# Kernel optimization log

Measured on AMD Instinct MI355X. Metric: run time of the kernel, lower is better.

The kernel has to match this reference:

```python
import jax, jax.numpy as jnp
import numpy as np

N = 20480      # total nodes
E = 327680     # total edges (avg degree 16)
B = 16         # graphs in batch
IN = 16        # node feature dim
H = 8          # hidden_out_channel
CO = 64        # conv_out_channel
ET = 36        # n_edge_types
EF = 2         # edge_features
OUT = 1        # classifier out
DIMS = [(IN, H), (H, H), (H, H), (H, CO)]


def setup_inputs() -> dict:
    key = jax.random.key(0)
    ks = jax.random.split(key, 32)
    inp = {}
    inp['x'] = jax.random.normal(ks[0], (N, IN), jnp.float32)
    inp['edge_index'] = jax.random.randint(ks[1], (2, E), 0, N)
    inp['edge_type'] = jax.random.randint(ks[2], (E,), 0, ET)
    inp['edge_attr'] = jax.random.normal(ks[3], (E, EF), jnp.float32)
    inp['cell_type'] = jax.random.randint(ks[4], (N,), 0, 2)
    inp['batch'] = (jnp.arange(N) // (N // B)).astype(jnp.int32)
    i = 5
    for l, (ci, co) in enumerate(DIMS, 1):
        d = ci * co
        s = 1.0 / np.sqrt(EF)
        inp[f'emb{l}'] = jax.random.normal(ks[i], (ET, d), jnp.float32) * 0.02; i += 1
        inp[f'wh{l}'] = jax.random.normal(ks[i], (EF, d), jnp.float32) * s; i += 1
        inp[f'bh{l}'] = jnp.zeros((d,), jnp.float32)
        inp[f'wg{l}'] = jax.random.normal(ks[i], (EF, d), jnp.float32) * s; i += 1
        inp[f'bg{l}'] = jnp.zeros((d,), jnp.float32)
        inp[f'root{l}'] = jax.random.normal(ks[i], (ci, co), jnp.float32) / np.sqrt(ci); i += 1
        inp[f'bias{l}'] = jnp.zeros((co,), jnp.float32)
    inp['clf_w'] = jax.random.normal(ks[i], (CO, OUT), jnp.float32) / np.sqrt(CO)
    inp['clf_b'] = jnp.zeros((OUT,), jnp.float32)
    return inp


def edge_weights(etype, ef, emb, wh, bh, wg, bg):
    # EdgeNN: relu(embedding(type) * fc_h(feat) + fc_g(feat)) -> [E, cin*cout]
    return jax.nn.relu(emb[etype] * (ef @ wh + bh) + (ef @ wg + bg))


def nnconv(h, src, dst, W, root, bias):
    # NNConv(aggr='mean', root_weight=True): gather src feats, per-edge matmul, scatter-mean
    cin, cout = root.shape
    msg = jnp.einsum('ei,eio->eo', h[src], W.reshape(-1, cin, cout))  # [E, cout]
    agg = jax.ops.segment_sum(msg, dst, num_segments=N)
    deg = jax.ops.segment_sum(jnp.ones_like(msg[:, 0]), dst, num_segments=N)
    return agg / jnp.maximum(deg, 1.0)[:, None] + h @ root + bias


def reference(x, edge_index, edge_type, edge_attr, cell_type, batch,
              emb1, wh1, bh1, wg1, bg1, root1, bias1,
              emb2, wh2, bh2, wg2, bg2, root2, bias2,
              emb3, wh3, bh3, wg3, bg3, root3, bias3,
              emb4, wh4, bh4, wg4, bg4, root4, bias4,
              clf_w, clf_b):
    src, dst = edge_index[0], edge_index[1]
    layers = [(emb1, wh1, bh1, wg1, bg1, root1, bias1),
              (emb2, wh2, bh2, wg2, bg2, root2, bias2),
              (emb3, wh3, bh3, wg3, bg3, root3, bias3),
              (emb4, wh4, bh4, wg4, bg4, root4, bias4)]
    h = x
    for (emb, wh, bh, wg, bg, root, bias) in layers:  # fixed 4 structurally-distinct layers
        W = edge_weights(edge_type, edge_attr, emb, wh, bh, wg, bg)
        h = jax.nn.relu(nnconv(h, src, dst, W, root, bias))
    # gated scatter-mean pooling over tumor cells (cell_type == 1)
    gate = (cell_type == 1).astype(jnp.int32)
    seg = gate * (batch.astype(jnp.int32) + 1)  # 0 = masked-out bucket
    pooled = jax.ops.segment_sum(h, seg, num_segments=B + 1)
    cnt = jax.ops.segment_sum(jnp.ones((h.shape[0],), h.dtype), seg, num_segments=B + 1)
    pooled = (pooled / jnp.maximum(cnt, 1.0)[:, None])[1:B + 1]  # [B, CO]
    return jax.nn.sigmoid(pooled @ clf_w + clf_b)  # hazards [B, OUT]
```

## Files before the change

### kernel.cpp

```cpp
#include <hip/hip_runtime.h>
#include <math.h>

#define NN 20480
#define NE 327680
#define NBATCH 16

typedef float v2f __attribute__((ext_vector_type(2)));

#if __has_builtin(__builtin_elementwise_max)
#define VMAX0(a) __builtin_elementwise_max((a), (v2f){0.f, 0.f})
#else
static __device__ __forceinline__ v2f VMAX0(v2f a) {
  v2f r; r.x = fmaxf(a.x, 0.f); r.y = fmaxf(a.y, 0.f); return r;
}
#endif

__global__ void hist_kernel(const int* __restrict__ dst, int* __restrict__ cnt) {
  int e = blockIdx.x * blockDim.x + threadIdx.x;
  if (e < NE) atomicAdd(&cnt[dst[e]], 1);
}

__global__ __launch_bounds__(1024) void scan_kernel(const int* __restrict__ cnt,
                                                    int* __restrict__ off,
                                                    int* __restrict__ cur) {
  __shared__ int part[1024];
  int tid = threadIdx.x;
  const int PT = NN / 1024;
  int loc[PT];
  int run = 0;
  int base = tid * PT;
#pragma unroll
  for (int k = 0; k < PT; k++) { loc[k] = run; run += cnt[base + k]; }
  part[tid] = run;
  __syncthreads();
  for (int d = 1; d < 1024; d <<= 1) {
    int t = (tid >= d) ? part[tid - d] : 0;
    __syncthreads();
    part[tid] += t;
    __syncthreads();
  }
  int pre = (tid == 0) ? 0 : part[tid - 1];
#pragma unroll
  for (int k = 0; k < PT; k++) {
    off[base + k] = pre + loc[k];
    cur[base + k] = pre + loc[k];
  }
  if (tid == 1023) off[NN] = pre + run;
}

__global__ void scatter_kernel(const int* __restrict__ src, const int* __restrict__ dst,
                               const int* __restrict__ etype, const float* __restrict__ eattr,
                               int* __restrict__ cur, float4* __restrict__ es) {
  int e = blockIdx.x * blockDim.x + threadIdx.x;
  if (e >= NE) return;
  int d = dst[e];
  int pos = atomicAdd(&cur[d], 1);
  es[pos] = make_float4(__int_as_float(src[e]), __int_as_float(etype[e]),
                        eattr[2 * e], eattr[2 * e + 1]);
}

__global__ __launch_bounds__(256) void transpose_kernel(
    const float* __restrict__ e1, const float* __restrict__ e2,
    const float* __restrict__ e3, const float* __restrict__ e4,
    float* __restrict__ t1, float* __restrict__ t2,
    float* __restrict__ t3, float* __restrict__ t4) {
  int idx = blockIdx.x * 256 + threadIdx.x;
  if (idx < 36 * 128) {
    int t = idx >> 7, r = idx & 127, o = r >> 4, i = r & 15;
    t1[idx] = e1[(t << 7) + i * 8 + o];
  }
  if (idx < 36 * 64) {
    int t = idx >> 6, r = idx & 63, o = r >> 3, i = r & 7;
    t2[idx] = e2[(t << 6) + i * 8 + o];
    t3[idx] = e3[(t << 6) + i * 8 + o];
  }
  {
    int t = idx >> 9, r = idx & 511, o = r >> 3, i = r & 7;
    t4[idx] = e4[(t << 9) + i * 64 + o];
  }
}

__global__ __launch_bounds__(256) void layer_small16(
    const int* __restrict__ off, const float4* __restrict__ es,
    const float* __restrict__ h_in, const float* __restrict__ embT,
    const float* __restrict__ wh, const float* __restrict__ bh,
    const float* __restrict__ wg, const float* __restrict__ bg,
    const float* __restrict__ root, const float* __restrict__ bias,
    float* __restrict__ h_out) {
  constexpr int D = 128;
  int lane = threadIdx.x & 63;
  int o = lane & 7;
  int ihalf = (lane >> 3) & 1;
  int esub = lane >> 4;
  int ibase = ihalf * 8;
  v2f rwh0[4], rwh1[4], rbh[4], rwg0[4], rwg1[4], rbg[4], rroot[4];
#pragma unroll
  for (int p = 0; p < 4; p++) {
    int a = (ibase + 2 * p) * 8 + o, b = (ibase + 2 * p + 1) * 8 + o;
    rwh0[p] = (v2f){wh[a], wh[b]};
    rwh1[p] = (v2f){wh[D + a], wh[D + b]};
    rbh[p]  = (v2f){bh[a], bh[b]};
    rwg0[p] = (v2f){wg[a], wg[b]};
    rwg1[p] = (v2f){wg[D + a], wg[D + b]};
    rbg[p]  = (v2f){bg[a], bg[b]};
    rroot[p] = (v2f){root[a], root[b]};
  }
  float rbias = bias[o];
  int n = __builtin_amdgcn_readfirstlane((int)(blockIdx.x * 4) + (int)(threadIdx.x >> 6));
  int beg = off[n], end = off[n + 1];
  int nIter = (end - beg + 3) >> 2;
  float acc = 0.f;
  int j = beg + esub;
  bool val0 = j < end;
  float4 rec0 = val0 ? es[j] : make_float4(0.f, 0.f, 0.f, 0.f);
  int s0 = __float_as_int(rec0.x);
  const float4* hp0 = (const float4*)(h_in + s0 * 16 + ibase);
  float4 hA0 = hp0[0], hB0 = hp0[1];
  for (int it = 0; it < nIter; ++it) {
    int j1 = j + 4;
    bool val1 = j1 < end;
    float4 rec1 = val1 ? es[j1] : make_float4(0.f, 0.f, 0.f, 0.f);
    int s1 = __float_as_int(rec1.x);
    const float4* hp1 = (const float4*)(h_in + s1 * 16 + ibase);
    float4 hA1 = hp1[0], hB1 = hp1[1];
    int t0 = __float_as_int(rec0.y);
    const float4* sp = (const float4*)(embT + t0 * 128 + o * 16 + ibase);
    float4 sv0 = sp[0], sv1 = sp[1];
    v2f stv[4] = {(v2f){sv0.x, sv0.y}, (v2f){sv0.z, sv0.w},
                  (v2f){sv1.x, sv1.y}, (v2f){sv1.z, sv1.w}};
    v2f hv[4] = {(v2f){hA0.x, hA0.y}, (v2f){hA0.z, hA0.w},
                 (v2f){hB0.x, hB0.y}, (v2f){hB0.z, hB0.w}};
    v2f ef0 = (v2f){rec0.z, rec0.z}, ef1 = (v2f){rec0.w, rec0.w};
    v2f msg = {0.f, 0.f};
#pragma unroll
    for (int p = 0; p < 4; p++) {
      v2f hval = ef0 * rwh0[p] + ef1 * rwh1[p] + rbh[p];
      v2f gval = ef0 * rwg0[p] + ef1 * rwg1[p] + rbg[p];
      msg += hv[p] * VMAX0(stv[p] * hval + gval);
    }
    acc += val0 ? (msg.x + msg.y) : 0.f;
    rec0 = rec1; hA0 = hA1; hB0 = hB1; val0 = val1; j = j1;
  }
  acc += __shfl_xor(acc, 8);
  acc += __shfl_xor(acc, 16);
  acc += __shfl_xor(acc, 32);
  const float* hn = h_in + n * 16 + ibase;
  v2f rtv = {0.f, 0.f};
#pragma unroll
  for (int p = 0; p < 4; p++)
    rtv += (v2f){hn[2 * p], hn[2 * p + 1]} * rroot[p];
  float rt = rtv.x + rtv.y;
  rt += __shfl_xor(rt, 8);
  float deg = (float)(end - beg);
  float val = fmaxf(rbias + rt + acc / fmaxf(deg, 1.f), 0.f);
  if (lane < 8) h_out[n * 8 + o] = val;
}

__global__ __launch_bounds__(256) void layer_small8(
    const int* __restrict__ off, const float4* __restrict__ es,
    const float* __restrict__ h_in, const float* __restrict__ embT,
    const float* __restrict__ wh, const float* __restrict__ bh,
    const float* __restrict__ wg, const float* __restrict__ bg,
    const float* __restrict__ root, const float* __restrict__ bias,
    float* __restrict__ h_out) {
  int lane = threadIdx.x & 63;
  int o = lane & 7, esub = lane >> 3;
  v2f rwh0[4], rwh1[4], rbh[4], rwg0[4], rwg1[4], rbg[4], rroot[4];
#pragma unroll
  for (int p = 0; p < 4; p++) {
    int a = (2 * p) * 8 + o, b = (2 * p + 1) * 8 + o;
    rwh0[p] = (v2f){wh[a], wh[b]};
    rwh1[p] = (v2f){wh[64 + a], wh[64 + b]};
    rbh[p]  = (v2f){bh[a], bh[b]};
    rwg0[p] = (v2f){wg[a], wg[b]};
    rwg1[p] = (v2f){wg[64 + a], wg[64 + b]};
    rbg[p]  = (v2f){bg[a], bg[b]};
    rroot[p] = (v2f){root[a], root[b]};
  }
  float rbias = bias[o];
  int n = __builtin_amdgcn_readfirstlane((int)(blockIdx.x * 4) + (int)(threadIdx.x >> 6));
  int beg = off[n], end = off[n + 1];
  int nIter = (end - beg + 7) >> 3;
  float acc = 0.f;
  int j = beg + esub;
  bool val0 = j < end;
  float4 rec0 = val0 ? es[j] : make_float4(0.f, 0.f, 0.f, 0.f);
  int s0 = __float_as_int(rec0.x);
  const float4* hp0 = (const float4*)(h_in + s0 * 8);
  float4 hA0 = hp0[0], hB0 = hp0[1];
  for (int it = 0; it < nIter; ++it) {
    int j1 = j + 8;
    bool val1 = j1 < end;
    float4 rec1 = val1 ? es[j1] : make_float4(0.f, 0.f, 0.f, 0.f);
    int s1 = __float_as_int(rec1.x);
    const float4* hp1 = (const float4*)(h_in + s1 * 8);
    float4 hA1 = hp1[0], hB1 = hp1[1];
    int t0 = __float_as_int(rec0.y);
    const float4* sp = (const float4*)(embT + t0 * 64 + o * 8);
    float4 sv0 = sp[0], sv1 = sp[1];
    v2f stv[4] = {(v2f){sv0.x, sv0.y}, (v2f){sv0.z, sv0.w},
                  (v2f){sv1.x, sv1.y}, (v2f){sv1.z, sv1.w}};
    v2f hv[4] = {(v2f){hA0.x, hA0.y}, (v2f){hA0.z, hA0.w},
                 (v2f){hB0.x, hB0.y}, (v2f){hB0.z, hB0.w}};
    v2f ef0 = (v2f){rec0.z, rec0.z}, ef1 = (v2f){rec0.w, rec0.w};
    v2f msg = {0.f, 0.f};
#pragma unroll
    for (int p = 0; p < 4; p++) {
      v2f hval = ef0 * rwh0[p] + ef1 * rwh1[p] + rbh[p];
      v2f gval = ef0 * rwg0[p] + ef1 * rwg1[p] + rbg[p];
      msg += hv[p] * VMAX0(stv[p] * hval + gval);
    }
    acc += val0 ? (msg.x + msg.y) : 0.f;
    rec0 = rec1; hA0 = hA1; hB0 = hB1; val0 = val1; j = j1;
  }
  acc += __shfl_xor(acc, 8);
  acc += __shfl_xor(acc, 16);
  acc += __shfl_xor(acc, 32);
  const float* hn = h_in + n * 8;
  v2f rtv = {0.f, 0.f};
#pragma unroll
  for (int p = 0; p < 4; p++)
    rtv += (v2f){hn[2 * p], hn[2 * p + 1]} * rroot[p];
  float deg = (float)(end - beg);
  float val = fmaxf(rbias + rtv.x + rtv.y + acc / fmaxf(deg, 1.f), 0.f);
  if (lane < 8) h_out[n * 8 + o] = val;
}

__global__ __launch_bounds__(256) void layer_l4(
    const int* __restrict__ off, const float4* __restrict__ es,
    const float* __restrict__ h_in, const float* __restrict__ embT,
    const float* __restrict__ wh, const float* __restrict__ bh,
    const float* __restrict__ wg, const float* __restrict__ bg,
    const float* __restrict__ root, const float* __restrict__ bias,
    float* __restrict__ h_out) {
  int lane = threadIdx.x & 63;
  v2f rwh0[4], rwh1[4], rbh[4], rwg0[4], rwg1[4], rbg[4], rroot[4];
#pragma unroll
  for (int p = 0; p < 4; p++) {
    int a = (2 * p) * 64 + lane, b = (2 * p + 1) * 64 + lane;
    rwh0[p] = (v2f){wh[a], wh[b]};
    rwh1[p] = (v2f){wh[512 + a], wh[512 + b]};
    rbh[p]  = (v2f){bh[a], bh[b]};
    rwg0[p] = (v2f){wg[a], wg[b]};
    rwg1[p] = (v2f){wg[512 + a], wg[512 + b]};
    rbg[p]  = (v2f){bg[a], bg[b]};
    rroot[p] = (v2f){root[a], root[b]};
  }
  float rbias = bias[lane];
  int n = __builtin_amdgcn_readfirstlane((int)(blockIdx.x * 4) + (int)(threadIdx.x >> 6));
  int beg = off[n], end = off[n + 1];
  float acc0 = 0.f, acc1 = 0.f;
  int e = beg;
  for (; e + 2 <= end; e += 2) {
    float4 r0 = es[e], r1 = es[e + 1];
    int s0 = __float_as_int(r0.x), t0 = __float_as_int(r0.y);
    int s1 = __float_as_int(r1.x), t1 = __float_as_int(r1.y);
    const float4* hp0 = (const float4*)(h_in + s0 * 8);
    const float4* hp1 = (const float4*)(h_in + s1 * 8);
    float4 a0 = hp0[0], a1 = hp0[1];
    float4 b0 = hp1[0], b1 = hp1[1];
    const float4* ep0 = (const float4*)(embT + t0 * 512 + lane * 8);
    const float4* ep1 = (const float4*)(embT + t1 * 512 + lane * 8);
    float4 s00 = ep0[0], s01 = ep0[1];
    float4 s10 = ep1[0], s11 = ep1[1];
    v2f sv0[4] = {(v2f){s00.x, s00.y}, (v2f){s00.z, s00.w},
                  (v2f){s01.x, s01.y}, (v2f){s01.z, s01.w}};
    v2f sv1[4] = {(v2f){s10.x, s10.y}, (v2f){s10.z, s10.w},
                  (v2f){s11.x, s11.y}, (v2f){s11.z, s11.w}};
    v2f hva[4] = {(v2f){a0.x, a0.y}, (v2f){a0.z, a0.w},
                  (v2f){a1.x, a1.y}, (v2f){a1.z, a1.w}};
    v2f hvb[4] = {(v2f){b0.x, b0.y}, (v2f){b0.z, b0.w},
                  (v2f){b1.x, b1.y}, (v2f){b1.z, b1.w}};
    v2f e00 = (v2f){r0.z, r0.z}, e01 = (v2f){r0.w, r0.w};
    v2f e10 = (v2f){r1.z, r1.z}, e11 = (v2f){r1.w, r1.w};
    v2f m0 = {0.f, 0.f}, m1 = {0.f, 0.f};
#pragma unroll
    for (int p = 0; p < 4; p++) {
      v2f hv0 = e00 * rwh0[p] + e01 * rwh1[p] + rbh[p];
      v2f gv0 = e00 * rwg0[p] + e01 * rwg1[p] + rbg[p];
      m0 += hva[p] * VMAX0(sv0[p] * hv0 + gv0);
      v2f hv1 = e10 * rwh0[p] + e11 * rwh1[p] + rbh[p];
      v2f gv1 = e10 * rwg0[p] + e11 * rwg1[p] + rbg[p];
      m1 += hvb[p] * VMAX0(sv1[p] * hv1 + gv1);
    }
    acc0 += m0.x + m0.y;
    acc1 += m1.x + m1.y;
  }
  if (e < end) {
    float4 r0 = es[e];
    int s0 = __float_as_int(r0.x), t0 = __float_as_int(r0.y);
    const float4* hp0 = (const float4*)(h_in + s0 * 8);
    float4 a0 = hp0[0], a1 = hp0[1];
    const float4* ep0 = (const float4*)(embT + t0 * 512 + lane * 8);
    float4 s00 = ep0[0], s01 = ep0[1];
    v2f sv0[4] = {(v2f){s00.x, s00.y}, (v2f){s00.z, s00.w},
                  (v2f){s01.x, s01.y}, (v2f){s01.z, s01.w}};
    v2f hva[4] = {(v2f){a0.x, a0.y}, (v2f){a0.z, a0.w},
                  (v2f){a1.x, a1.y}, (v2f){a1.z, a1.w}};
    v2f e00 = (v2f){r0.z, r0.z}, e01 = (v2f){r0.w, r0.w};
    v2f m0 = {0.f, 0.f};
#pragma unroll
    for (int p = 0; p < 4; p++) {
      v2f hv0 = e00 * rwh0[p] + e01 * rwh1[p] + rbh[p];
      v2f gv0 = e00 * rwg0[p] + e01 * rwg1[p] + rbg[p];
      m0 += hva[p] * VMAX0(sv0[p] * hv0 + gv0);
    }
    acc0 += m0.x + m0.y;
  }
  float acc = acc0 + acc1;
  float deg = (float)(end - beg);
  const float* hn = h_in + n * 8;
  v2f rtv = {0.f, 0.f};
#pragma unroll
  for (int p = 0; p < 4; p++)
    rtv += (v2f){hn[2 * p], hn[2 * p + 1]} * rroot[p];
  h_out[n * 64 + lane] = fmaxf(rbias + rtv.x + rtv.y + acc / fmaxf(deg, 1.f), 0.f);
}

__global__ __launch_bounds__(256) void pool1_kernel(
    const float* __restrict__ h4, const int* __restrict__ ct,
    float* __restrict__ pooled, float* __restrict__ pcnt) {
  __shared__ float ss[4][64];
  __shared__ float sc[4];
  int b = blockIdx.x / 20, c = blockIdx.x % 20;
  int base = b * (NN / NBATCH) + c * 64;
  int o = threadIdx.x & 63, sub = threadIdx.x >> 6;
  float sum = 0.f, cnt = 0.f;
  for (int j = sub; j < 64; j += 4) {
    int n = base + j;
    if (ct[n] == 1) { sum += h4[n * 64 + o]; cnt += 1.f; }
  }
  ss[sub][o] = sum;
  if (o == 0) sc[sub] = cnt;
  __syncthreads();
  if (threadIdx.x < 64) {
    float tot = ss[0][o] + ss[1][o] + ss[2][o] + ss[3][o];
    unsafeAtomicAdd(&pooled[b * 64 + o], tot);
    if (o == 0) unsafeAtomicAdd(&pcnt[b], sc[0] + sc[1] + sc[2] + sc[3]);
  }
}

__global__ __launch_bounds__(1024) void pool2_kernel(
    const float* __restrict__ pooled, const float* __restrict__ pcnt,
    const float* __restrict__ clf_w, const float* __restrict__ clf_b,
    float* __restrict__ out) {
  int b = threadIdx.x >> 6, o = threadIdx.x & 63;
  float c = pcnt[b];
  float v = (pooled[b * 64 + o] / fmaxf(c, 1.f)) * clf_w[o];
#pragma unroll
  for (int d = 32; d; d >>= 1) v += __shfl_down(v, d);
  if (o == 0) out[b] = 1.f / (1.f + expf(-(v + clf_b[0])));
}

extern "C" void kernel_launch(void* const* d_in, const int* in_sizes, int n_in,
                              void* d_out, int out_size, void* d_ws, size_t ws_size,
                              hipStream_t stream) {
  (void)in_sizes; (void)n_in; (void)out_size; (void)ws_size;
  const float* x     = (const float*)d_in[0];
  const int*   eidx  = (const int*)d_in[1];
  const int*   src   = eidx;
  const int*   dst   = eidx + NE;
  const int*   etype = (const int*)d_in[2];
  const float* eattr = (const float*)d_in[3];
  const int*   ct    = (const int*)d_in[4];
  const float *emb[4], *wh[4], *bh[4], *wg[4], *bg[4], *root[4], *bias[4];
  for (int l = 0; l < 4; l++) {
    int b0 = 6 + 7 * l;
    emb[l]  = (const float*)d_in[b0 + 0];
    wh[l]   = (const float*)d_in[b0 + 1];
    bh[l]   = (const float*)d_in[b0 + 2];
    wg[l]   = (const float*)d_in[b0 + 3];
    bg[l]   = (const float*)d_in[b0 + 4];
    root[l] = (const float*)d_in[b0 + 5];
    bias[l] = (const float*)d_in[b0 + 6];
  }
  const float* clf_w = (const float*)d_in[34];
  const float* clf_b = (const float*)d_in[35];
  float* outp = (float*)d_out;

  float* ws  = (float*)d_ws;
  int*    off    = (int*)ws;
  float4* es     = (float4*)(ws + 20484);
  float*  hA     = ws + 20484 + 4 * NE;
  float*  hB     = hA + 8 * NN;
  float*  h4     = hB + 8 * NN;
  float*  embT1  = h4 + 64 * NN;
  float*  embT2  = embT1 + 36 * 128;
  float*  embT3  = embT2 + 36 * 64;
  float*  embT4  = embT3 + 36 * 64;
  float*  pooled = embT4 + 36 * 512;
  float*  pcnt   = pooled + 16 * 64;
  int*    cnt    = (int*)h4;
  int*    cur    = cnt + NN;

  hipMemsetAsync(cnt, 0, NN * sizeof(int), stream);
  hipMemsetAsync(pooled, 0, (16 * 64 + 16) * sizeof(float), stream);
  hist_kernel<<<NE / 256, 256, 0, stream>>>(dst, cnt);
  transpose_kernel<<<72, 256, 0, stream>>>(emb[0], emb[1], emb[2], emb[3],
                                           embT1, embT2, embT3, embT4);
  scan_kernel<<<1, 1024, 0, stream>>>(cnt, off, cur);
  scatter_kernel<<<NE / 256, 256, 0, stream>>>(src, dst, etype, eattr, cur, es);

  layer_small16<<<NN / 4, 256, 0, stream>>>(off, es, x, embT1,
      wh[0], bh[0], wg[0], bg[0], root[0], bias[0], hA);
  layer_small8<<<NN / 4, 256, 0, stream>>>(off, es, hA, embT2,
      wh[1], bh[1], wg[1], bg[1], root[1], bias[1], hB);
  layer_small8<<<NN / 4, 256, 0, stream>>>(off, es, hB, embT3,
      wh[2], bh[2], wg[2], bg[2], root[2], bias[2], hA);
  layer_l4<<<NN / 4, 256, 0, stream>>>(off, es, hA, embT4,
      wh[3], bh[3], wg[3], bg[3], root[3], bias[3], h4);

  pool1_kernel<<<320, 256, 0, stream>>>(h4, ct, pooled, pcnt);
  pool2_kernel<<<1, 1024, 0, stream>>>(pooled, pcnt, clf_w, clf_b, outp);
}
```

Baseline: 305.4 us.

## Fuse prep kernels, pack two nodes per wave, unroll layer4 edge loop

Measured after the change: 309.2 us. No clear change (+1.2%).

```diff
diff --git a/kernel.cpp b/kernel.cpp
--- a/kernel.cpp
+++ b/kernel.cpp
@@ -15,16 +15,41 @@
 }
 #endif
 
-__global__ void hist_kernel(const int* __restrict__ dst, int* __restrict__ cnt) {
-  int e = blockIdx.x * blockDim.x + threadIdx.x;
-  if (e < NE) atomicAdd(&cnt[dst[e]], 1);
+__global__ __launch_bounds__(256) void prep_kernel(
+    const int* __restrict__ dst, int* __restrict__ cnt,
+    const float* __restrict__ e1, const float* __restrict__ e2,
+    const float* __restrict__ e3, const float* __restrict__ e4,
+    float* __restrict__ t1, float* __restrict__ t2,
+    float* __restrict__ t3, float* __restrict__ t4) {
+  int b = blockIdx.x;
+  if (b < NE / 256) {
+    int e = b * 256 + threadIdx.x;
+    atomicAdd(&cnt[dst[e]], 1);
+  } else {
+    int idx = (b - NE / 256) * 256 + threadIdx.x;
+    if (idx < 36 * 128) {
+      int t = idx >> 7, r = idx & 127, o = r >> 4, i = r & 15;
+      t1[idx] = e1[(t << 7) + i * 8 + o];
+    }
+    if (idx < 36 * 64) {
+      int t = idx >> 6, r = idx & 63, o = r >> 3, i = r & 7;
+      t2[idx] = e2[(t << 6) + i * 8 + o];
+      t3[idx] = e3[(t << 6) + i * 8 + o];
+    }
+    {
+      int t = idx >> 9, r = idx & 511, o = r >> 3, i = r & 7;
+      t4[idx] = e4[(t << 9) + i * 64 + o];
+    }
+  }
 }
 
 __global__ __launch_bounds__(1024) void scan_kernel(const int* __restrict__ cnt,
                                                     int* __restrict__ off,
-                                                    int* __restrict__ cur) {
+                                                    int* __restrict__ cur,
+                                                    float* __restrict__ poolz) {
   __shared__ int part[1024];
   int tid = threadIdx.x;
+  if (tid < 16 * 64 + 16) poolz[tid] = 0.f;
   const int PT = NN / 1024;
   int loc[PT];
   int run = 0;
@@ -57,27 +82,6 @@
   int pos = atomicAdd(&cur[d], 1);
   es[pos] = make_float4(__int_as_float(src[e]), __int_as_float(etype[e]),
                         eattr[2 * e], eattr[2 * e + 1]);
-}
-
-__global__ __launch_bounds__(256) void transpose_kernel(
-    const float* __restrict__ e1, const float* __restrict__ e2,
-    const float* __restrict__ e3, const float* __restrict__ e4,
-    float* __restrict__ t1, float* __restrict__ t2,
-    float* __restrict__ t3, float* __restrict__ t4) {
-  int idx = blockIdx.x * 256 + threadIdx.x;
-  if (idx < 36 * 128) {
-    int t = idx >> 7, r = idx & 127, o = r >> 4, i = r & 15;
-    t1[idx] = e1[(t << 7) + i * 8 + o];
-  }
-  if (idx < 36 * 64) {
-    int t = idx >> 6, r = idx & 63, o = r >> 3, i = r & 7;
-    t2[idx] = e2[(t << 6) + i * 8 + o];
-    t3[idx] = e3[(t << 6) + i * 8 + o];
-  }
-  {
-    int t = idx >> 9, r = idx & 511, o = r >> 3, i = r & 7;
-    t4[idx] = e4[(t << 9) + i * 64 + o];
-  }
 }
 
 __global__ __launch_bounds__(256) void layer_small16(
@@ -108,7 +112,6 @@
   float rbias = bias[o];
   int n = __builtin_amdgcn_readfirstlane((int)(blockIdx.x * 4) + (int)(threadIdx.x >> 6));
   int beg = off[n], end = off[n + 1];
-  int nIter = (end - beg + 3) >> 2;
   float acc = 0.f;
   int j = beg + esub;
   bool val0 = j < end;
@@ -116,7 +119,7 @@
   int s0 = __float_as_int(rec0.x);
   const float4* hp0 = (const float4*)(h_in + s0 * 16 + ibase);
   float4 hA0 = hp0[0], hB0 = hp0[1];
-  for (int it = 0; it < nIter; ++it) {
+  while (__ballot(val0)) {
     int j1 = j + 4;
     bool val1 = j1 < end;
     float4 rec1 = val1 ? es[j1] : make_float4(0.f, 0.f, 0.f, 0.f);
@@ -164,7 +167,7 @@
     const float* __restrict__ root, const float* __restrict__ bias,
     float* __restrict__ h_out) {
   int lane = threadIdx.x & 63;
-  int o = lane & 7, esub = lane >> 3;
+  int o = lane & 7, esub = (lane >> 3) & 3, nsub = lane >> 5;
   v2f rwh0[4], rwh1[4], rbh[4], rwg0[4], rwg1[4], rbg[4], rroot[4];
 #pragma unroll
   for (int p = 0; p < 4; p++) {
@@ -178,9 +181,9 @@
     rroot[p] = (v2f){root[a], root[b]};
   }
   float rbias = bias[o];
-  int n = __builtin_amdgcn_readfirstlane((int)(blockIdx.x * 4) + (int)(threadIdx.x >> 6));
+  int wid = (int)(blockIdx.x * 4) + (int)(threadIdx.x >> 6);
+  int n = wid * 2 + nsub;
   int beg = off[n], end = off[n + 1];
-  int nIter = (end - beg + 7) >> 3;
   float acc = 0.f;
   int j = beg + esub;
   bool val0 = j < end;
@@ -188,8 +191,8 @@
   int s0 = __float_as_int(rec0.x);
   const float4* hp0 = (const float4*)(h_in + s0 * 8);
   float4 hA0 = hp0[0], hB0 = hp0[1];
-  for (int it = 0; it < nIter; ++it) {
-    int j1 = j + 8;
+  while (__ballot(val0)) {
+    int j1 = j + 4;
     bool val1 = j1 < end;
     float4 rec1 = val1 ? es[j1] : make_float4(0.f, 0.f, 0.f, 0.f);
     int s1 = __float_as_int(rec1.x);
@@ -215,7 +218,6 @@
   }
   acc += __shfl_xor(acc, 8);
   acc += __shfl_xor(acc, 16);
-  acc += __shfl_xor(acc, 32);
   const float* hn = h_in + n * 8;
   v2f rtv = {0.f, 0.f};
 #pragma unroll
@@ -223,7 +225,7 @@
     rtv += (v2f){hn[2 * p], hn[2 * p + 1]} * rroot[p];
   float deg = (float)(end - beg);
   float val = fmaxf(rbias + rtv.x + rtv.y + acc / fmaxf(deg, 1.f), 0.f);
-  if (lane < 8) h_out[n * 8 + o] = val;
+  if ((lane & 24) == 0) h_out[n * 8 + o] = val;
 }
 
 __global__ __launch_bounds__(256) void layer_l4(
@@ -250,62 +252,60 @@
   int n = __builtin_amdgcn_readfirstlane((int)(blockIdx.x * 4) + (int)(threadIdx.x >> 6));
   int beg = off[n], end = off[n + 1];
   float acc0 = 0.f, acc1 = 0.f;
+
+  auto edge_msg = [&](float4 r, float4 h0, float4 h1,
+                      float4 s0v, float4 s1v) -> float {
+    v2f ef0 = (v2f){r.z, r.z}, ef1 = (v2f){r.w, r.w};
+    v2f hv[4] = {(v2f){h0.x, h0.y}, (v2f){h0.z, h0.w},
+                 (v2f){h1.x, h1.y}, (v2f){h1.z, h1.w}};
+    v2f sv[4] = {(v2f){s0v.x, s0v.y}, (v2f){s0v.z, s0v.w},
+                 (v2f){s1v.x, s1v.y}, (v2f){s1v.z, s1v.w}};
+    v2f m = {0.f, 0.f};
+#pragma unroll
+    for (int p = 0; p < 4; p++) {
+      v2f hval = ef0 * rwh0[p] + ef1 * rwh1[p] + rbh[p];
+      v2f gval = ef0 * rwg0[p] + ef1 * rwg1[p] + rbg[p];
+      m += hv[p] * VMAX0(sv[p] * hval + gval);
+    }
+    return m.x + m.y;
+  };
+
   int e = beg;
-  for (; e + 2 <= end; e += 2) {
-    float4 r0 = es[e], r1 = es[e + 1];
+  for (; e + 4 <= end; e += 4) {
+    float4 r0 = es[e], r1 = es[e + 1], r2 = es[e + 2], r3 = es[e + 3];
     int s0 = __float_as_int(r0.x), t0 = __float_as_int(r0.y);
     int s1 = __float_as_int(r1.x), t1 = __float_as_int(r1.y);
+    int s2 = __float_as_int(r2.x), t2 = __float_as_int(r2.y);
+    int s3 = __float_as_int(r3.x), t3 = __float_as_int(r3.y);
     const float4* hp0 = (const float4*)(h_in + s0 * 8);
     const float4* hp1 = (const float4*)(h_in + s1 * 8);
+    const float4* hp2 = (const float4*)(h_in + s2 * 8);
+    const float4* hp3 = (const float4*)(h_in + s3 * 8);
     float4 a0 = hp0[0], a1 = hp0[1];
     float4 b0 = hp1[0], b1 = hp1[1];
+    float4 c0 = hp2[0], c1 = hp2[1];
+    float4 d0 = hp3[0], d1 = hp3[1];
     const float4* ep0 = (const float4*)(embT + t0 * 512 + lane * 8);
     const float4* ep1 = (const float4*)(embT + t1 * 512 + lane * 8);
+    const float4* ep2 = (const float4*)(embT + t2 * 512 + lane * 8);
+    const float4* ep3 = (const float4*)(embT + t3 * 512 + lane * 8);
     float4 s00 = ep0[0], s01 = ep0[1];
     float4 s10 = ep1[0], s11 = ep1[1];
-    v2f sv0[4] = {(v2f){s00.x, s00.y}, (v2f){s00.z, s00.w},
-                  (v2f){s01.x, s01.y}, (v2f){s01.z, s01.w}};
-    v2f sv1[4] = {(v2f){s10.x, s10.y}, (v2f){s10.z, s10.w},
-                  (v2f){s11.x, s11.y}, (v2f){s11.z, s11.w}};
-    v2f hva[4] = {(v2f){a0.x, a0.y}, (v2f){a0.z, a0.w},
-                  (v2f){a1.x, a1.y}, (v2f){a1.z, a1.w}};
-    v2f hvb[4] = {(v2f){b0.x, b0.y}, (v2f){b0.z, b0.w},
-                  (v2f){b1.x, b1.y}, (v2f){b1.z, b1.w}};
-    v2f e00 = (v2f){r0.z, r0.z}, e01 = (v2f){r0.w, r0.w};
-    v2f e10 = (v2f){r1.z, r1.z}, e11 = (v2f){r1.w, r1.w};
-    v2f m0 = {0.f, 0.f}, m1 = {0.f, 0.f};
-#pragma unroll
-    for (int p = 0; p < 4; p++) {
-      v2f hv0 = e00 * rwh0[p] + e01 * rwh1[p] + rbh[p];
-      v2f gv0 = e00 * rwg0[p] + e01 * rwg1[p] + rbg[p];
-      m0 += hva[p] * VMAX0(sv0[p] * hv0 + gv0);
-      v2f hv1 = e10 * rwh0[p] + e11 * rwh1[p] + rbh[p];
-      v2f gv1 = e10 * rwg0[p] + e11 * rwg1[p] + rbg[p];
-      m1 += hvb[p] * VMAX0(sv1[p] * hv1 + gv1);
-    }
-    acc0 += m0.x + m0.y;
-    acc1 += m1.x + m1.y;
-  }
-  if (e < end) {
+    float4 s20 = ep2[0], s21 = ep2[1];
+    float4 s30 = ep3[0], s31 = ep3[1];
+    acc0 += edge_msg(r0, a0, a1, s00, s01);
+    acc1 += edge_msg(r1, b0, b1, s10, s11);
+    acc0 += edge_msg(r2, c0, c1, s20, s21);
+    acc1 += edge_msg(r3, d0, d1, s30, s31);
+  }
+  for (; e < end; ++e) {
     float4 r0 = es[e];
     int s0 = __float_as_int(r0.x), t0 = __float_as_int(r0.y);
     const float4* hp0 = (const float4*)(h_in + s0 * 8);
     float4 a0 = hp0[0], a1 = hp0[1];
     const float4* ep0 = (const float4*)(embT + t0 * 512 + lane * 8);
     float4 s00 = ep0[0], s01 = ep0[1];
-    v2f sv0[4] = {(v2f){s00.x, s00.y}, (v2f){s00.z, s00.w},
-                  (v2f){s01.x, s01.y}, (v2f){s01.z, s01.w}};
-    v2f hva[4] = {(v2f){a0.x, a0.y}, (v2f){a0.z, a0.w},
-                  (v2f){a1.x, a1.y}, (v2f){a1.z, a1.w}};
-    v2f e00 = (v2f){r0.z, r0.z}, e01 = (v2f){r0.w, r0.w};
-    v2f m0 = {0.f, 0.f};
-#pragma unroll
-    for (int p = 0; p < 4; p++) {
-      v2f hv0 = e00 * rwh0[p] + e01 * rwh1[p] + rbh[p];
-      v2f gv0 = e00 * rwg0[p] + e01 * rwg1[p] + rbg[p];
-      m0 += hva[p] * VMAX0(sv0[p] * hv0 + gv0);
-    }
-    acc0 += m0.x + m0.y;
+    acc0 += edge_msg(r0, a0, a1, s00, s01);
   }
   float acc = acc0 + acc1;
   float deg = (float)(end - beg);
@@ -394,18 +394,16 @@
   int*    cur    = cnt + NN;
 
   hipMemsetAsync(cnt, 0, NN * sizeof(int), stream);
-  hipMemsetAsync(pooled, 0, (16 * 64 + 16) * sizeof(float), stream);
-  hist_kernel<<<NE / 256, 256, 0, stream>>>(dst, cnt);
-  transpose_kernel<<<72, 256, 0, stream>>>(emb[0], emb[1], emb[2], emb[3],
-                                           embT1, embT2, embT3, embT4);
-  scan_kernel<<<1, 1024, 0, stream>>>(cnt, off, cur);
+  prep_kernel<<<NE / 256 + 72, 256, 0, stream>>>(dst, cnt, emb[0], emb[1], emb[2], emb[3],
+                                                 embT1, embT2, embT3, embT4);
+  scan_kernel<<<1, 1024, 0, stream>>>(cnt, off, cur, pooled);
   scatter_kernel<<<NE / 256, 256, 0, stream>>>(src, dst, etype, eattr, cur, es);
 
   layer_small16<<<NN / 4, 256, 0, stream>>>(off, es, x, embT1,
       wh[0], bh[0], wg[0], bg[0], root[0], bias[0], hA);
-  layer_small8<<<NN / 4, 256, 0, stream>>>(off, es, hA, embT2,
+  layer_small8<<<NN / 8, 256, 0, stream>>>(off, es, hA, embT2,
       wh[1], bh[1], wg[1], bg[1], root[1], bias[1], hB);
-  layer_small8<<<NN / 4, 256, 0, stream>>>(off, es, hB, embT3,
+  layer_small8<<<NN / 8, 256, 0, stream>>>(off, es, hB, embT3,
       wh[2], bh[2], wg[2], bg[2], root[2], bias[2], hA);
   layer_l4<<<NN / 4, 256, 0, stream>>>(off, es, hA, embT4,
       wh[3], bh[3], wg[3], bg[3], root[3], bias[3], h4);
```

## Fuse prep kernels, pack two nodes per wave, prefetch edges in layer 4

Applied to the files above, without the earlier changes.

After: 335.9 us. 1.1x slower.

```diff
diff --git a/kernel.cpp b/kernel.cpp
--- a/kernel.cpp
+++ b/kernel.cpp
@@ -7,24 +7,45 @@
 
 typedef float v2f __attribute__((ext_vector_type(2)));
 
-#if __has_builtin(__builtin_elementwise_max)
-#define VMAX0(a) __builtin_elementwise_max((a), (v2f){0.f, 0.f})
-#else
-static __device__ __forceinline__ v2f VMAX0(v2f a) {
+static __device__ __forceinline__ v2f vmax0(v2f a) {
   v2f r; r.x = fmaxf(a.x, 0.f); r.y = fmaxf(a.y, 0.f); return r;
 }
-#endif
-
-__global__ void hist_kernel(const int* __restrict__ dst, int* __restrict__ cnt) {
-  int e = blockIdx.x * blockDim.x + threadIdx.x;
-  if (e < NE) atomicAdd(&cnt[dst[e]], 1);
+
+__global__ __launch_bounds__(256) void prep_kernel(
+    const int* __restrict__ dst, int* __restrict__ cnt,
+    const float* __restrict__ e1, const float* __restrict__ e2,
+    const float* __restrict__ e3, const float* __restrict__ e4,
+    float* __restrict__ t1, float* __restrict__ t2,
+    float* __restrict__ t3, float* __restrict__ t4) {
+  int b = blockIdx.x;
+  if (b < NE / 256) {
+    int e = b * 256 + threadIdx.x;
+    atomicAdd(&cnt[dst[e]], 1);
+  } else {
+    int idx = (b - NE / 256) * 256 + threadIdx.x;
+    if (idx < 36 * 128) {
+      int t = idx >> 7, r = idx & 127, o = r >> 4, i = r & 15;
+      t1[idx] = e1[(t << 7) + i * 8 + o];
+    }
+    if (idx < 36 * 64) {
+      int t = idx >> 6, r = idx & 63, o = r >> 3, i = r & 7;
+      t2[idx] = e2[(t << 6) + i * 8 + o];
+      t3[idx] = e3[(t << 6) + i * 8 + o];
+    }
+    {
+      int t = idx >> 9, r = idx & 511, o = r >> 3, i = r & 7;
+      t4[idx] = e4[(t << 9) + i * 64 + o];
+    }
+  }
 }
 
 __global__ __launch_bounds__(1024) void scan_kernel(const int* __restrict__ cnt,
                                                     int* __restrict__ off,
-                                                    int* __restrict__ cur) {
+                                                    int* __restrict__ cur,
+                                                    float* __restrict__ poolz) {
   __shared__ int part[1024];
   int tid = threadIdx.x;
+  if (tid < 16 * 64 + 16) poolz[tid] = 0.f;
   const int PT = NN / 1024;
   int loc[PT];
   int run = 0;
@@ -57,27 +78,6 @@
   int pos = atomicAdd(&cur[d], 1);
   es[pos] = make_float4(__int_as_float(src[e]), __int_as_float(etype[e]),
                         eattr[2 * e], eattr[2 * e + 1]);
-}
-
-__global__ __launch_bounds__(256) void transpose_kernel(
-    const float* __restrict__ e1, const float* __restrict__ e2,
-    const float* __restrict__ e3, const float* __restrict__ e4,
-    float* __restrict__ t1, float* __restrict__ t2,
-    float* __restrict__ t3, float* __restrict__ t4) {
-  int idx = blockIdx.x * 256 + threadIdx.x;
-  if (idx < 36 * 128) {
-    int t = idx >> 7, r = idx & 127, o = r >> 4, i = r & 15;
-    t1[idx] = e1[(t << 7) + i * 8 + o];
-  }
-  if (idx < 36 * 64) {
-    int t = idx >> 6, r = idx & 63, o = r >> 3, i = r & 7;
-    t2[idx] = e2[(t << 6) + i * 8 + o];
-    t3[idx] = e3[(t << 6) + i * 8 + o];
-  }
-  {
-    int t = idx >> 9, r = idx & 511, o = r >> 3, i = r & 7;
-    t4[idx] = e4[(t << 9) + i * 64 + o];
-  }
 }
 
 __global__ __launch_bounds__(256) void layer_small16(
@@ -108,7 +108,6 @@
   float rbias = bias[o];
   int n = __builtin_amdgcn_readfirstlane((int)(blockIdx.x * 4) + (int)(threadIdx.x >> 6));
   int beg = off[n], end = off[n + 1];
-  int nIter = (end - beg + 3) >> 2;
   float acc = 0.f;
   int j = beg + esub;
   bool val0 = j < end;
@@ -116,7 +115,7 @@
   int s0 = __float_as_int(rec0.x);
   const float4* hp0 = (const float4*)(h_in + s0 * 16 + ibase);
   float4 hA0 = hp0[0], hB0 = hp0[1];
-  for (int it = 0; it < nIter; ++it) {
+  while (__ballot(val0)) {
     int j1 = j + 4;
     bool val1 = j1 < end;
     float4 rec1 = val1 ? es[j1] : make_float4(0.f, 0.f, 0.f, 0.f);
@@ -136,7 +135,7 @@
     for (int p = 0; p < 4; p++) {
       v2f hval = ef0 * rwh0[p] + ef1 * rwh1[p] + rbh[p];
       v2f gval = ef0 * rwg0[p] + ef1 * rwg1[p] + rbg[p];
-      msg += hv[p] * VMAX0(stv[p] * hval + gval);
+      msg += hv[p] * vmax0(stv[p] * hval + gval);
     }
     acc += val0 ? (msg.x + msg.y) : 0.f;
     rec0 = rec1; hA0 = hA1; hB0 = hB1; val0 = val1; j = j1;
@@ -164,7 +163,7 @@
     const float* __restrict__ root, const float* __restrict__ bias,
     float* __restrict__ h_out) {
   int lane = threadIdx.x & 63;
-  int o = lane & 7, esub = lane >> 3;
+  int o = lane & 7, esub = (lane >> 3) & 3, nsub = lane >> 5;
   v2f rwh0[4], rwh1[4], rbh[4], rwg0[4], rwg1[4], rbg[4], rroot[4];
 #pragma unroll
   for (int p = 0; p < 4; p++) {
@@ -178,9 +177,9 @@
     rroot[p] = (v2f){root[a], root[b]};
   }
   float rbias = bias[o];
-  int n = __builtin_amdgcn_readfirstlane((int)(blockIdx.x * 4) + (int)(threadIdx.x >> 6));
+  int wid = (int)(blockIdx.x * 4) + (int)(threadIdx.x >> 6);
+  int n = wid * 2 + nsub;
   int beg = off[n], end = off[n + 1];
-  int nIter = (end - beg + 7) >> 3;
   float acc = 0.f;
   int j = beg + esub;
   bool val0 = j < end;
@@ -188,8 +187,8 @@
   int s0 = __float_as_int(rec0.x);
   const float4* hp0 = (const float4*)(h_in + s0 * 8);
   float4 hA0 = hp0[0], hB0 = hp0[1];
-  for (int it = 0; it < nIter; ++it) {
-    int j1 = j + 8;
+  while (__ballot(val0)) {
+    int j1 = j + 4;
     bool val1 = j1 < end;
     float4 rec1 = val1 ? es[j1] : make_float4(0.f, 0.f, 0.f, 0.f);
     int s1 = __float_as_int(rec1.x);
@@ -208,14 +207,13 @@
     for (int p = 0; p < 4; p++) {
       v2f hval = ef0 * rwh0[p] + ef1 * rwh1[p] + rbh[p];
       v2f gval = ef0 * rwg0[p] + ef1 * rwg1[p] + rbg[p];
-      msg += hv[p] * VMAX0(stv[p] * hval + gval);
+      msg += hv[p] * vmax0(stv[p] * hval + gval);
     }
     acc += val0 ? (msg.x + msg.y) : 0.f;
     rec0 = rec1; hA0 = hA1; hB0 = hB1; val0 = val1; j = j1;
   }
   acc += __shfl_xor(acc, 8);
   acc += __shfl_xor(acc, 16);
-  acc += __shfl_xor(acc, 32);
   const float* hn = h_in + n * 8;
   v2f rtv = {0.f, 0.f};
 #pragma unroll
@@ -223,7 +221,7 @@
     rtv += (v2f){hn[2 * p], hn[2 * p + 1]} * rroot[p];
   float deg = (float)(end - beg);
   float val = fmaxf(rbias + rtv.x + rtv.y + acc / fmaxf(deg, 1.f), 0.f);
-  if (lane < 8) h_out[n * 8 + o] = val;
+  if ((lane & 24) == 0) h_out[n * 8 + o] = val;
 }
 
 __global__ __launch_bounds__(256) void layer_l4(
@@ -234,7 +232,7 @@
     const float* __restrict__ root, const float* __restrict__ bias,
     float* __restrict__ h_out) {
   int lane = threadIdx.x & 63;
-  v2f rwh0[4], rwh1[4], rbh[4], rwg0[4], rwg1[4], rbg[4], rroot[4];
+  v2f rwh0[4], rwh1[4], rbh[4], rwg0[4], rwg1[4], rbg[4];
 #pragma unroll
   for (int p = 0; p < 4; p++) {
     int a = (2 * p) * 64 + lane, b = (2 * p + 1) * 64 + lane;
@@ -244,33 +242,22 @@
     rwg0[p] = (v2f){wg[a], wg[b]};
     rwg1[p] = (v2f){wg[512 + a], wg[512 + b]};
     rbg[p]  = (v2f){bg[a], bg[b]};
-    rroot[p] = (v2f){root[a], root[b]};
-  }
-  float rbias = bias[lane];
-  int n = __builtin_amdgcn_readfirstlane((int)(blockIdx.x * 4) + (int)(threadIdx.x >> 6));
+  }
+  int n = (int)(blockIdx.x * 4) + (int)(threadIdx.x >> 6);
   int beg = off[n], end = off[n + 1];
   float acc0 = 0.f, acc1 = 0.f;
-  int e = beg;
-  for (; e + 2 <= end; e += 2) {
-    float4 r0 = es[e], r1 = es[e + 1];
-    int s0 = __float_as_int(r0.x), t0 = __float_as_int(r0.y);
-    int s1 = __float_as_int(r1.x), t1 = __float_as_int(r1.y);
-    const float4* hp0 = (const float4*)(h_in + s0 * 8);
-    const float4* hp1 = (const float4*)(h_in + s1 * 8);
-    float4 a0 = hp0[0], a1 = hp0[1];
-    float4 b0 = hp1[0], b1 = hp1[1];
-    const float4* ep0 = (const float4*)(embT + t0 * 512 + lane * 8);
-    const float4* ep1 = (const float4*)(embT + t1 * 512 + lane * 8);
-    float4 s00 = ep0[0], s01 = ep0[1];
-    float4 s10 = ep1[0], s11 = ep1[1];
+
+  auto pair_compute = [&](float4 r0, float4 r1,
+                          float4 h00, float4 h01, float4 h10, float4 h11,
+                          float4 s00, float4 s01, float4 s10, float4 s11) {
     v2f sv0[4] = {(v2f){s00.x, s00.y}, (v2f){s00.z, s00.w},
                   (v2f){s01.x, s01.y}, (v2f){s01.z, s01.w}};
     v2f sv1[4] = {(v2f){s10.x, s10.y}, (v2f){s10.z, s10.w},
                   (v2f){s11.x, s11.y}, (v2f){s11.z, s11.w}};
-    v2f hva[4] = {(v2f){a0.x, a0.y}, (v2f){a0.z, a0.w},
-                  (v2f){a1.x, a1.y}, (v2f){a1.z, a1.w}};
-    v2f hvb[4] = {(v2f){b0.x, b0.y}, (v2f){b0.z, b0.w},
-                  (v2f){b1.x, b1.y}, (v2f){b1.z, b1.w}};
+    v2f hva[4] = {(v2f){h00.x, h00.y}, (v2f){h00.z, h00.w},
+                  (v2f){h01.x, h01.y}, (v2f){h01.z, h01.w}};
+    v2f hvb[4] = {(v2f){h10.x, h10.y}, (v2f){h10.z, h10.w},
+                  (v2f){h11.x, h11.y}, (v2f){h11.z, h11.w}};
     v2f e00 = (v2f){r0.z, r0.z}, e01 = (v2f){r0.w, r0.w};
     v2f e10 = (v2f){r1.z, r1.z}, e11 = (v2f){r1.w, r1.w};
     v2f m0 = {0.f, 0.f}, m1 = {0.f, 0.f};
@@ -278,16 +265,49 @@
     for (int p = 0; p < 4; p++) {
       v2f hv0 = e00 * rwh0[p] + e01 * rwh1[p] + rbh[p];
       v2f gv0 = e00 * rwg0[p] + e01 * rwg1[p] + rbg[p];
-      m0 += hva[p] * VMAX0(sv0[p] * hv0 + gv0);
+      m0 += hva[p] * vmax0(sv0[p] * hv0 + gv0);
       v2f hv1 = e10 * rwh0[p] + e11 * rwh1[p] + rbh[p];
       v2f gv1 = e10 * rwg0[p] + e11 * rwg1[p] + rbg[p];
-      m1 += hvb[p] * VMAX0(sv1[p] * hv1 + gv1);
+      m1 += hvb[p] * vmax0(sv1[p] * hv1 + gv1);
     }
     acc0 += m0.x + m0.y;
     acc1 += m1.x + m1.y;
-  }
-  if (e < end) {
-    float4 r0 = es[e];
+  };
+
+  int npair = (end - beg) >> 1;
+  int e = beg;
+  float4 rC0, rC1, hC00, hC01, hC10, hC11, sC00, sC01, sC10, sC11;
+  if (npair > 0) {
+    rC0 = es[e]; rC1 = es[e + 1];
+    int s0 = __float_as_int(rC0.x), t0 = __float_as_int(rC0.y);
+    int s1 = __float_as_int(rC1.x), t1 = __float_as_int(rC1.y);
+    const float4* hp0 = (const float4*)(h_in + s0 * 8);
+    const float4* hp1 = (const float4*)(h_in + s1 * 8);
+    const float4* ep0 = (const float4*)(embT + t0 * 512 + lane * 8);
+    const float4* ep1 = (const float4*)(embT + t1 * 512 + lane * 8);
+    hC00 = hp0[0]; hC01 = hp0[1]; hC10 = hp1[0]; hC11 = hp1[1];
+    sC00 = ep0[0]; sC01 = ep0[1]; sC10 = ep1[0]; sC11 = ep1[1];
+  }
+  for (int it = 0; it < npair; ++it) {
+    bool more = (it + 1) < npair;
+    float4 rN0, rN1;
+    if (more) { rN0 = es[e + 2]; rN1 = es[e + 3]; }
+    pair_compute(rC0, rC1, hC00, hC01, hC10, hC11, sC00, sC01, sC10, sC11);
+    if (more) {
+      int s0 = __float_as_int(rN0.x), t0 = __float_as_int(rN0.y);
+      int s1 = __float_as_int(rN1.x), t1 = __float_as_int(rN1.y);
+      const float4* hp0 = (const float4*)(h_in + s0 * 8);
+      const float4* hp1 = (const float4*)(h_in + s1 * 8);
+      const float4* ep0 = (const float4*)(embT + t0 * 512 + lane * 8);
+      const float4* ep1 = (const float4*)(embT + t1 * 512 + lane * 8);
+      hC00 = hp0[0]; hC01 = hp0[1]; hC10 = hp1[0]; hC11 = hp1[1];
+      sC00 = ep0[0]; sC01 = ep0[1]; sC10 = ep1[0]; sC11 = ep1[1];
+      rC0 = rN0; rC1 = rN1;
+    }
+    e += 2;
+  }
+  for (int ee = beg + 2 * npair; ee < end; ++ee) {
+    float4 r0 = es[ee];
     int s0 = __float_as_int(r0.x), t0 = __float_as_int(r0.y);
     const float4* hp0 = (const float4*)(h_in + s0 * 8);
     float4 a0 = hp0[0], a1 = hp0[1];
@@ -303,18 +323,17 @@
     for (int p = 0; p < 4; p++) {
       v2f hv0 = e00 * rwh0[p] + e01 * rwh1[p] + rbh[p];
       v2f gv0 = e00 * rwg0[p] + e01 * rwg1[p] + rbg[p];
-      m0 += hva[p] * VMAX0(sv0[p] * hv0 + gv0);
+      m0 += hva[p] * vmax0(sv0[p] * hv0 + gv0);
     }
     acc0 += m0.x + m0.y;
   }
   float acc = acc0 + acc1;
   float deg = (float)(end - beg);
   const float* hn = h_in + n * 8;
-  v2f rtv = {0.f, 0.f};
-#pragma unroll
-  for (int p = 0; p < 4; p++)
-    rtv += (v2f){hn[2 * p], hn[2 * p + 1]} * rroot[p];
-  h_out[n * 64 + lane] = fmaxf(rbias + rtv.x + rtv.y + acc / fmaxf(deg, 1.f), 0.f);
+  float rt = bias[lane];
+#pragma unroll
+  for (int i = 0; i < 8; i++) rt = fmaf(hn[i], root[i * 64 + lane], rt);
+  h_out[n * 64 + lane] = fmaxf(rt + acc / fmaxf(deg, 1.f), 0.f);
 }
 
 __global__ __launch_bounds__(256) void pool1_kernel(
@@ -394,18 +413,16 @@
   int*    cur    = cnt + NN;
 
   hipMemsetAsync(cnt, 0, NN * sizeof(int), stream);
-  hipMemsetAsync(pooled, 0, (16 * 64 + 16) * sizeof(float), stream);
-  hist_kernel<<<NE / 256, 256, 0, stream>>>(dst, cnt);
-  transpose_kernel<<<72, 256, 0, stream>>>(emb[0], emb[1], emb[2], emb[3],
-                                           embT1, embT2, embT3, embT4);
-  scan_kernel<<<1, 1024, 0, stream>>>(cnt, off, cur);
+  prep_kernel<<<NE / 256 + 72, 256, 0, stream>>>(dst, cnt, emb[0], emb[1], emb[2], emb[3],
+                                                 embT1, embT2, embT3, embT4);
+  scan_kernel<<<1, 1024, 0, stream>>>(cnt, off, cur, pooled);
   scatter_kernel<<<NE / 256, 256, 0, stream>>>(src, dst, etype, eattr, cur, es);
 
   layer_small16<<<NN / 4, 256, 0, stream>>>(off, es, x, embT1,
       wh[0], bh[0], wg[0], bg[0], root[0], bias[0], hA);
-  layer_small8<<<NN / 4, 256, 0, stream>>>(off, es, hA, embT2,
+  layer_small8<<<NN / 8, 256, 0, stream>>>(off, es, hA, embT2,
       wh[1], bh[1], wg[1], bg[1], root[1], bias[1], hB);
-  layer_small8<<<NN / 4, 256, 0, stream>>>(off, es, hB, embT3,
+  layer_small8<<<NN / 8, 256, 0, stream>>>(off, es, hB, embT3,
       wh[2], bh[2], wg[2], bg[2], root[2], bias[2], hA);
   layer_l4<<<NN / 4, 256, 0, stream>>>(off, es, hA, embT4,
       wh[3], bh[3], wg[3], bg[3], root[3], bias[3], h4);
```
